# Kernel tuning notes

Measured on AMD Instinct MI355X. Metric: run time of the kernel, lower is better.

## Reference

```python
import jax, jax.numpy as jnp
import numpy as np

H = 4            # num_heads (forced: 128 projection / d_k=32)
DK = 32          # hardcoded d_k
SCALE = 1.0 / np.sqrt(32.0)
EPS = 1e-5       # LayerNorm eps (torch default)


def setup_inputs() -> dict:
    key = jax.random.key(0)
    ks = jax.random.split(key, 8)
    B, L, Dq, Dkv, M = 16, 4096, 512, 512, 512
    def w(k, shape, fan_in):
        return (jax.random.normal(k, shape, jnp.float32) / np.sqrt(fan_in)).astype(jnp.float32)
    return {
        "Q_in":  jax.random.normal(ks[0], (B, L, Dq),  jnp.float32),
        "KV_in": jax.random.normal(ks[1], (B, L, Dkv), jnp.float32),
        "Wq":  w(ks[2], (Dq, 128), Dq),   "bq":  jnp.zeros((128,), jnp.float32),
        "Wk":  w(ks[3], (Dkv, 128), Dkv), "bk":  jnp.zeros((128,), jnp.float32),
        "Wv":  w(ks[4], (Dkv, 128), Dkv), "bv":  jnp.zeros((128,), jnp.float32),
        "Wo":  w(ks[5], (128, M), 128),   "bo":  jnp.zeros((M,), jnp.float32),
        "Wqo": w(ks[6], (128, M), 128),   "bqo": jnp.zeros((M,), jnp.float32),
        "gamma": jnp.ones((M,), jnp.float32),
        "beta":  jnp.zeros((M,), jnp.float32),
    }


def reference(Q_in, KV_in, Wq, bq, Wk, bk, Wv, bv, Wo, bo, Wqo, bqo, gamma, beta):
    B, L, _ = Q_in.shape
    Qm = Q_in @ Wq + bq          # (B, L, 128)
    Km = KV_in @ Wk + bk         # (B, L, 128)
    Vm = KV_in @ Wv + bv         # (B, L, 128)

    def heads(X):
        # view(B, L, H, DK).permute(0, 2, 3, 1) -> (B, H, DK, L)
        return X.reshape(B, L, H, DK).transpose(0, 2, 3, 1)

    Qh, Kh, Vh = heads(Qm), heads(Km), heads(Vm)
    # matmul contracts over the SEQUENCE dim -> feature-feature scores (B,H,DK,DK)
    scores = jnp.einsum('bhdl,bhel->bhde', Qh, Kh) * SCALE
    attn = jax.nn.softmax(scores, axis=-1)          # dropout = identity (eval)
    out_h = jnp.einsum('bhde,bhel->bhdl', attn, Vh)  # (B, H, DK, L)
    out_h = out_h.transpose(0, 3, 1, 2).reshape(B, L, H * DK)  # (B, L, 128)

    out = out_h @ Wo + bo        # (B, L, M)
    Qm_ = Qm @ Wqo + bqo         # (B, L, M)
    x = Qm_ + out
    mu = jnp.mean(x, axis=-1, keepdims=True)
    var = jnp.var(x, axis=-1, keepdims=True)
    y = (x - mu) * jax.lax.rsqrt(var + EPS) * gamma + beta
    return (y, attn)
```

## Files before the change

kernel.cpp:

```cpp
#include <hip/hip_runtime.h>
#include <hip/hip_bf16.h>

typedef __bf16 bf16x8 __attribute__((ext_vector_type(8)));
typedef float  f32x4  __attribute__((ext_vector_type(4)));

#define SCALE_QK 0.17677669529663687f
#define LDSS 40

__device__ __forceinline__ float b2f(ushort u) {
    __hip_bfloat16 h; *reinterpret_cast<ushort*>(&h) = u; return __bfloat162float(h);
}
__device__ __forceinline__ ushort f2b(float f) {
    __hip_bfloat16 h = __float2bfloat16(f); return *reinterpret_cast<ushort*>(&h);
}

__global__ void k_prep(const float* __restrict__ Wq, const float* __restrict__ Wk,
                       const float* __restrict__ Wv, const float* __restrict__ Wqo,
                       const float* __restrict__ Wo,
                       ushort* __restrict__ WqThi, ushort* __restrict__ WqTlo,
                       ushort* __restrict__ WkThi, ushort* __restrict__ WkTlo,
                       ushort* __restrict__ WvT,  ushort* __restrict__ WqoT,
                       ushort* __restrict__ WoB) {
    int idx = blockIdx.x * 256 + threadIdx.x;
    int mat = idx >> 16, i = idx & 65535;
    if (mat == 0) {
        int n = i >> 9, k = i & 511;
        float w = Wq[k * 128 + n];
        ushort hi = f2b(w);
        WqThi[i] = hi; WqTlo[i] = f2b(w - b2f(hi));
    } else if (mat == 1) {
        int n = i >> 9, k = i & 511;
        float w = Wk[k * 128 + n];
        ushort hi = f2b(w);
        WkThi[i] = hi; WkTlo[i] = f2b(w - b2f(hi));
    } else if (mat == 2) {
        int n = i >> 9, k = i & 511;
        WvT[i] = f2b(Wv[k * 128 + n]);
    } else if (mat == 3) {
        int n = i >> 7, k = i & 127;
        WqoT[i] = f2b(Wqo[k * 512 + n]);
    } else if (mat == 4) {
        WoB[i] = f2b(Wo[i]);
    }
}

__global__ __launch_bounds__(256) void k_proj_split(
        const float* __restrict__ A, const ushort* __restrict__ BThi,
        const ushort* __restrict__ BTlo, const float* __restrict__ bias,
        float* __restrict__ outF, ushort* __restrict__ outB) {
    __shared__ __align__(16) ushort AsH[128 * LDSS], AsL[128 * LDSS];
    __shared__ __align__(16) ushort BsH[128 * LDSS], BsL[128 * LDSS];
    const int row0 = blockIdx.x * 128;
    const int tid  = threadIdx.x;
    const int wid  = tid >> 6, lane = tid & 63;
    const int wm = wid >> 1, wn = wid & 1;
    const int quad = lane >> 4, l16 = lane & 15;
    const int sr = tid >> 2;
    const int sc = (tid & 3) * 8;

    f32x4 acc[4][4] = {};

    for (int k0 = 0; k0 < 512; k0 += 32) {
        __syncthreads();
#pragma unroll
        for (int p = 0; p < 2; ++p) {
            int r = sr + p * 64;
            float4 a0 = *(const float4*)&A[(size_t)(row0 + r) * 512 + k0 + sc];
            float4 a1 = *(const float4*)&A[(size_t)(row0 + r) * 512 + k0 + sc + 4];
            float av[8] = {a0.x, a0.y, a0.z, a0.w, a1.x, a1.y, a1.z, a1.w};
            union { uint4 v; ushort u[8]; } H, L;
#pragma unroll
            for (int i = 0; i < 8; ++i) {
                ushort hi = f2b(av[i]);
                H.u[i] = hi;
                L.u[i] = f2b(av[i] - b2f(hi));
            }
            *(uint4*)&AsH[r * LDSS + sc] = H.v;
            *(uint4*)&AsL[r * LDSS + sc] = L.v;
            *(uint4*)&BsH[r * LDSS + sc] = *(const uint4*)&BThi[(size_t)r * 512 + k0 + sc];
            *(uint4*)&BsL[r * LDSS + sc] = *(const uint4*)&BTlo[(size_t)r * 512 + k0 + sc];
        }
        __syncthreads();
        bf16x8 aH[4], aL[4];
#pragma unroll
        for (int i = 0; i < 4; ++i) {
            int ro = (wm * 64 + i * 16 + l16) * LDSS + quad * 8;
            aH[i] = *reinterpret_cast<const bf16x8*>(&AsH[ro]);
            aL[i] = *reinterpret_cast<const bf16x8*>(&AsL[ro]);
        }
#pragma unroll
        for (int j = 0; j < 4; ++j) {
            int ro = (wn * 64 + j * 16 + l16) * LDSS + quad * 8;
            bf16x8 bH = *reinterpret_cast<const bf16x8*>(&BsH[ro]);
            bf16x8 bL = *reinterpret_cast<const bf16x8*>(&BsL[ro]);
#pragma unroll
            for (int i = 0; i < 4; ++i) {
                acc[i][j] = __builtin_amdgcn_mfma_f32_16x16x32_bf16(aL[i], bH, acc[i][j], 0, 0, 0);
                acc[i][j] = __builtin_amdgcn_mfma_f32_16x16x32_bf16(aH[i], bL, acc[i][j], 0, 0, 0);
                acc[i][j] = __builtin_amdgcn_mfma_f32_16x16x32_bf16(aH[i], bH, acc[i][j], 0, 0, 0);
            }
        }
    }

#pragma unroll
    for (int i = 0; i < 4; ++i)
#pragma unroll
        for (int j = 0; j < 4; ++j) {
            int ncol = wn * 64 + j * 16 + l16;
            float bv = bias[ncol];
#pragma unroll
            for (int r = 0; r < 4; ++r) {
                int mrow = row0 + wm * 64 + i * 16 + quad * 4 + r;
                float v = acc[i][j][r] + bv;
                if (outF) outF[(size_t)mrow * 128 + ncol] = v;
                if (outB) outB[(size_t)mrow * 128 + ncol] = f2b(v);
            }
        }
}

__global__ __launch_bounds__(256) void k_proj_kv(
        const float* __restrict__ A,
        const ushort* __restrict__ BKhi, const ushort* __restrict__ BKlo,
        const ushort* __restrict__ BV,
        const float* __restrict__ biasK, const float* __restrict__ biasV,
        float* __restrict__ KmF, ushort* __restrict__ VmB) {
    __shared__ __align__(16) ushort AsH[128 * LDSS], AsL[128 * LDSS];
    __shared__ __align__(16) ushort BsKH[128 * LDSS], BsKL[128 * LDSS], BsV[128 * LDSS];
    const int row0 = blockIdx.x * 128;
    const int tid  = threadIdx.x;
    const int wid  = tid >> 6, lane = tid & 63;
    const int wm = wid >> 1, wn = wid & 1;
    const int quad = lane >> 4, l16 = lane & 15;
    const int sr = tid >> 2;
    const int sc = (tid & 3) * 8;

    f32x4 accK[4][4] = {};
    f32x4 accV[4][4] = {};

    for (int k0 = 0; k0 < 512; k0 += 32) {
        __syncthreads();
#pragma unroll
        for (int p = 0; p < 2; ++p) {
            int r = sr + p * 64;
            float4 a0 = *(const float4*)&A[(size_t)(row0 + r) * 512 + k0 + sc];
            float4 a1 = *(const float4*)&A[(size_t)(row0 + r) * 512 + k0 + sc + 4];
            float av[8] = {a0.x, a0.y, a0.z, a0.w, a1.x, a1.y, a1.z, a1.w};
            union { uint4 v; ushort u[8]; } H, L;
#pragma unroll
            for (int i = 0; i < 8; ++i) {
                ushort hi = f2b(av[i]);
                H.u[i] = hi;
                L.u[i] = f2b(av[i] - b2f(hi));
            }
            *(uint4*)&AsH[r * LDSS + sc] = H.v;
            *(uint4*)&AsL[r * LDSS + sc] = L.v;
            *(uint4*)&BsKH[r * LDSS + sc] = *(const uint4*)&BKhi[(size_t)r * 512 + k0 + sc];
            *(uint4*)&BsKL[r * LDSS + sc] = *(const uint4*)&BKlo[(size_t)r * 512 + k0 + sc];
            *(uint4*)&BsV [r * LDSS + sc] = *(const uint4*)&BV  [(size_t)r * 512 + k0 + sc];
        }
        __syncthreads();
        bf16x8 aH[4], aL[4];
#pragma unroll
        for (int i = 0; i < 4; ++i) {
            int ro = (wm * 64 + i * 16 + l16) * LDSS + quad * 8;
            aH[i] = *reinterpret_cast<const bf16x8*>(&AsH[ro]);
            aL[i] = *reinterpret_cast<const bf16x8*>(&AsL[ro]);
        }
#pragma unroll
        for (int j = 0; j < 4; ++j) {
            int ro = (wn * 64 + j * 16 + l16) * LDSS + quad * 8;
            bf16x8 bKH = *reinterpret_cast<const bf16x8*>(&BsKH[ro]);
            bf16x8 bKL = *reinterpret_cast<const bf16x8*>(&BsKL[ro]);
            bf16x8 bV  = *reinterpret_cast<const bf16x8*>(&BsV [ro]);
#pragma unroll
            for (int i = 0; i < 4; ++i) {
                accK[i][j] = __builtin_amdgcn_mfma_f32_16x16x32_bf16(aL[i], bKH, accK[i][j], 0, 0, 0);
                accK[i][j] = __builtin_amdgcn_mfma_f32_16x16x32_bf16(aH[i], bKL, accK[i][j], 0, 0, 0);
                accK[i][j] = __builtin_amdgcn_mfma_f32_16x16x32_bf16(aH[i], bKH, accK[i][j], 0, 0, 0);
                accV[i][j] = __builtin_amdgcn_mfma_f32_16x16x32_bf16(aH[i], bV,  accV[i][j], 0, 0, 0);
            }
        }
    }

#pragma unroll
    for (int i = 0; i < 4; ++i)
#pragma unroll
        for (int j = 0; j < 4; ++j) {
            int ncol = wn * 64 + j * 16 + l16;
            float bk = biasK[ncol], bv = biasV[ncol];
#pragma unroll
            for (int r = 0; r < 4; ++r) {
                int mrow = row0 + wm * 64 + i * 16 + quad * 4 + r;
                KmF[(size_t)mrow * 128 + ncol] = accK[i][j][r] + bk;
                VmB[(size_t)mrow * 128 + ncol] = f2b(accV[i][j][r] + bv);
            }
        }
}

__global__ __launch_bounds__(256) void k_scores(
        const float* __restrict__ Qm, const float* __restrict__ Km,
        float* __restrict__ partial) {
    int b = blockIdx.x, sp = blockIdx.y;
    int t = threadIdx.x;
    int h = t >> 6, tl = t & 63;
    int d0 = (tl >> 3) * 4, e0 = (tl & 7) * 4;
    const float* Qb = Qm + ((size_t)b * 4096 + sp * 128) * 128 + h * 32 + d0;
    const float* Kb = Km + ((size_t)b * 4096 + sp * 128) * 128 + h * 32 + e0;
    float acc[4][4] = {};
#pragma unroll 4
    for (int l = 0; l < 128; ++l) {
        float4 q4 = *(const float4*)(Qb + (size_t)l * 128);
        float4 k4 = *(const float4*)(Kb + (size_t)l * 128);
        float q[4] = {q4.x, q4.y, q4.z, q4.w};
        float k[4] = {k4.x, k4.y, k4.z, k4.w};
#pragma unroll
        for (int i = 0; i < 4; ++i)
#pragma unroll
            for (int j = 0; j < 4; ++j) acc[i][j] += q[i] * k[j];
    }
    float* P = partial + ((size_t)(sp * 64 + b * 4 + h)) * 1024;
#pragma unroll
    for (int i = 0; i < 4; ++i)
#pragma unroll
        for (int j = 0; j < 4; ++j)
            P[(d0 + i) * 32 + e0 + j] = acc[i][j];
}

__global__ __launch_bounds__(256) void k_attn(
        const float* __restrict__ partial, const ushort* __restrict__ WoB,
        float* __restrict__ attnOut, ushort* __restrict__ WcT) {
    int bh = blockIdx.x; int b = bh >> 2, h = bh & 3;
    __shared__ float aS[1024];
    __shared__ __align__(16) ushort wS[32 * 512];
    int t = threadIdx.x;
    for (int i = t; i < 1024; i += 256) {
        float s = 0.f;
#pragma unroll
        for (int sp = 0; sp < 32; ++sp)
            s += partial[(size_t)(sp * 64 + bh) * 1024 + i];
        aS[i] = s * SCALE_QK;
    }
    for (int i = t; i < 2048; i += 256) {
        int r = i >> 6, c = (i & 63) * 8;
        *(uint4*)&wS[r * 512 + c] = *(const uint4*)&WoB[(size_t)(h * 32 + r) * 512 + c];
    }
    __syncthreads();
    if (t < 32) {
        float m = -1e30f;
#pragma unroll
        for (int e = 0; e < 32; ++e) m = fmaxf(m, aS[t * 32 + e]);
        float p[32]; float sum = 0.f;
#pragma unroll
        for (int e = 0; e < 32; ++e) { p[e] = __expf(aS[t * 32 + e] - m); sum += p[e]; }
        float inv = 1.f / sum;
#pragma unroll
        for (int e = 0; e < 32; ++e) aS[t * 32 + e] = p[e] * inv;
    }
    __syncthreads();
    for (int i = t; i < 1024; i += 256)
        attnOut[(size_t)bh * 1024 + i] = aS[i];
    int e = t & 31, mg = t >> 5;
    for (int mi = 0; mi < 64; ++mi) {
        int m = mg * 64 + mi;
        float acc = 0.f;
#pragma unroll
        for (int d = 0; d < 32; ++d)
            acc += aS[d * 32 + e] * b2f(wS[d * 512 + m]);
        WcT[((size_t)b * 512 + m) * 128 + h * 32 + e] = f2b(acc);
    }
}

__global__ __launch_bounds__(256) void k_out_ln(
        const ushort* __restrict__ Vm, const ushort* __restrict__ Qm,
        const ushort* __restrict__ WcT, const ushort* __restrict__ WqoT,
        const float* __restrict__ bo, const float* __restrict__ bqo,
        const float* __restrict__ gamma, const float* __restrict__ beta,
        float* __restrict__ Y) {
    __shared__ __align__(16) ushort As[64 * LDSS];
    __shared__ __align__(16) ushort Bs[512 * LDSS];
    __shared__ float sumS[4][64], sumSS[4][64], muA[64], rsA[64];
    const int row0 = blockIdx.x * 64;
    const int b = row0 >> 12;
    const ushort* WcTb = WcT + (size_t)b * 512 * 128;
    const int tid = threadIdx.x;
    const int wid = tid >> 6, lane = tid & 63;
    const int quad = lane >> 4, l16 = lane & 15;
    const int sr = tid >> 2;
    const int sc = (tid & 3) * 8;

    f32x4 acc[4][8] = {};

    for (int k0 = 0; k0 < 256; k0 += 32) {
        const ushort* Asrc; const ushort* Bsrc; int kk;
        if (k0 < 128) { Asrc = Vm; Bsrc = WcTb; kk = k0; }
        else          { Asrc = Qm; Bsrc = WqoT; kk = k0 - 128; }
        __syncthreads();
        *(uint4*)&As[sr * LDSS + sc] =
            *(const uint4*)&Asrc[(size_t)(row0 + sr) * 128 + kk + sc];
#pragma unroll
        for (int p = 0; p < 8; ++p) {
            int r = sr + p * 64;
            *(uint4*)&Bs[r * LDSS + sc] = *(const uint4*)&Bsrc[(size_t)r * 128 + kk + sc];
        }
        __syncthreads();
        bf16x8 aF[4];
#pragma unroll
        for (int i = 0; i < 4; ++i)
            aF[i] = *reinterpret_cast<const bf16x8*>(&As[(i * 16 + l16) * LDSS + quad * 8]);
#pragma unroll
        for (int j = 0; j < 8; ++j) {
            bf16x8 bF = *reinterpret_cast<const bf16x8*>(
                &Bs[(wid * 128 + j * 16 + l16) * LDSS + quad * 8]);
#pragma unroll
            for (int i = 0; i < 4; ++i)
                acc[i][j] = __builtin_amdgcn_mfma_f32_16x16x32_bf16(aF[i], bF, acc[i][j], 0, 0, 0);
        }
    }

    float bv[8];
#pragma unroll
    for (int j = 0; j < 8; ++j) {
        int ncol = wid * 128 + j * 16 + l16;
        bv[j] = bo[ncol] + bqo[ncol];
    }
    float sArr[4][4], ssArr[4][4];
#pragma unroll
    for (int i = 0; i < 4; ++i)
#pragma unroll
        for (int r = 0; r < 4; ++r) {
            float s = 0.f, ss = 0.f;
#pragma unroll
            for (int j = 0; j < 8; ++j) {
                float x = acc[i][j][r] + bv[j];
                s += x; ss += x * x;
            }
            sArr[i][r] = s; ssArr[i][r] = ss;
        }
#pragma unroll
    for (int off = 1; off < 16; off <<= 1)
#pragma unroll
        for (int i = 0; i < 4; ++i)
#pragma unroll
            for (int r = 0; r < 4; ++r) {
                sArr[i][r]  += __shfl_xor(sArr[i][r],  off, 64);
                ssArr[i][r] += __shfl_xor(ssArr[i][r], off, 64);
            }
    if (l16 == 0) {
#pragma unroll
        for (int i = 0; i < 4; ++i)
#pragma unroll
            for (int r = 0; r < 4; ++r) {
                int row = i * 16 + quad * 4 + r;
                sumS[wid][row]  = sArr[i][r];
                sumSS[wid][row] = ssArr[i][r];
            }
    }
    __syncthreads();
    if (tid < 64) {
        float s = sumS[0][tid] + sumS[1][tid] + sumS[2][tid] + sumS[3][tid];
        float ss = sumSS[0][tid] + sumSS[1][tid] + sumSS[2][tid] + sumSS[3][tid];
        float mu = s * (1.f / 512.f);
        float var = ss * (1.f / 512.f) - mu * mu;
        muA[tid] = mu;
        rsA[tid] = rsqrtf(var + 1e-5f);
    }
    __syncthreads();

    float gj[8], bj[8];
#pragma unroll
    for (int j = 0; j < 8; ++j) {
        int ncol = wid * 128 + j * 16 + l16;
        gj[j] = gamma[ncol]; bj[j] = beta[ncol];
    }
#pragma unroll
    for (int i = 0; i < 4; ++i)
#pragma unroll
        for (int r = 0; r < 4; ++r) {
            int row = i * 16 + quad * 4 + r;
            float mu = muA[row], rstd = rsA[row];
            size_t base = (size_t)(row0 + row) * 512 + wid * 128 + l16;
#pragma unroll
            for (int j = 0; j < 8; ++j) {
                float x = acc[i][j][r] + bv[j];
                Y[base + j * 16] = (x - mu) * rstd * gj[j] + bj[j];
            }
        }
}

extern "C" void kernel_launch(void* const* d_in, const int* in_sizes, int n_in,
                              void* d_out, int out_size, void* d_ws, size_t ws_size,
                              hipStream_t stream) {
    const float* Qin   = (const float*)d_in[0];
    const float* KVin  = (const float*)d_in[1];
    const float* Wq    = (const float*)d_in[2];
    const float* bq    = (const float*)d_in[3];
    const float* Wk    = (const float*)d_in[4];
    const float* bk    = (const float*)d_in[5];
    const float* Wv    = (const float*)d_in[6];
    const float* bv    = (const float*)d_in[7];
    const float* Wo    = (const float*)d_in[8];
    const float* bo    = (const float*)d_in[9];
    const float* Wqo   = (const float*)d_in[10];
    const float* bqo   = (const float*)d_in[11];
    const float* gamma = (const float*)d_in[12];
    const float* beta  = (const float*)d_in[13];
    float* out = (float*)d_out;
    float* attnOut = out + 33554432;

    char* ws = (char*)d_ws;
    ushort* WqThi = (ushort*)(ws);
    ushort* WqTlo = (ushort*)(ws + 131072);
    ushort* WkThi = (ushort*)(ws + 262144);
    ushort* WkTlo = (ushort*)(ws + 393216);
    ushort* WvT   = (ushort*)(ws + 524288);
    ushort* WqoT  = (ushort*)(ws + 655360);
    ushort* WoB   = (ushort*)(ws + 786432);
    float*  QmF   = (float*) (ws + 917504);
    float*  KmF   = (float*) (ws + 34471936);
    ushort* QmB   = (ushort*)(ws + 68026368);
    ushort* VmB   = (ushort*)(ws + 84803584);
    float*  part  = (float*) (ws + 101580800);
    ushort* WcT   = (ushort*)(ws + 109969408);

    k_prep<<<1280, 256, 0, stream>>>(Wq, Wk, Wv, Wqo, Wo,
                                     WqThi, WqTlo, WkThi, WkTlo, WvT, WqoT, WoB);
    k_proj_split<<<512, 256, 0, stream>>>(Qin, WqThi, WqTlo, bq, QmF, QmB);
    k_proj_kv<<<512, 256, 0, stream>>>(KVin, WkThi, WkTlo, WvT, bk, bv, KmF, VmB);
    k_scores<<<dim3(16, 32), 256, 0, stream>>>(QmF, KmF, part);
    k_attn<<<64, 256, 0, stream>>>(part, WoB, attnOut, WcT);
    k_out_ln<<<1024, 256, 0, stream>>>(VmB, QmB, WcT, WqoT, bo, bqo, gamma, beta, out);
}
```

Before: 488.7 us.

## Fuse Q/KV projections with score computation and switch split-bf16 to fp16 MFMA

Merges the Q projection, K/V projection and per-chunk QK^T score kernels into one kernel. Q and K tiles now stay in LDS as fp16 and feed MFMA score products directly, so the fp32 Qm/Km intermediates are no longer written to or read back from global memory. The three-term split-bf16 emulation of fp32 GEMMs is replaced with a single fp16 MFMA per tile, cutting matrix instructions and LDS staging. The cost is lower precision from fp16 inputs, with possible overflow or accuracy loss, and higher LDS use per block.

```diff
diff --git a/kernel.cpp b/kernel.cpp
--- a/kernel.cpp
+++ b/kernel.cpp
@@ -1,41 +1,41 @@
 #include <hip/hip_runtime.h>
 #include <hip/hip_bf16.h>
 
-typedef __bf16 bf16x8 __attribute__((ext_vector_type(8)));
-typedef float  f32x4  __attribute__((ext_vector_type(4)));
+typedef __bf16   bf16x8 __attribute__((ext_vector_type(8)));
+typedef _Float16 f16x8  __attribute__((ext_vector_type(8)));
+typedef float    f32x4  __attribute__((ext_vector_type(4)));
 
 #define SCALE_QK 0.17677669529663687f
 #define LDSS 40
+#define TL   136
 
 __device__ __forceinline__ float b2f(ushort u) {
     __hip_bfloat16 h; *reinterpret_cast<ushort*>(&h) = u; return __bfloat162float(h);
 }
 __device__ __forceinline__ ushort f2b(float f) {
     __hip_bfloat16 h = __float2bfloat16(f); return *reinterpret_cast<ushort*>(&h);
+}
+__device__ __forceinline__ ushort f2h(float f) {
+    union { _Float16 h; ushort u; } x; x.h = (_Float16)f; return x.u;
 }
 
 __global__ void k_prep(const float* __restrict__ Wq, const float* __restrict__ Wk,
                        const float* __restrict__ Wv, const float* __restrict__ Wqo,
                        const float* __restrict__ Wo,
-                       ushort* __restrict__ WqThi, ushort* __restrict__ WqTlo,
-                       ushort* __restrict__ WkThi, ushort* __restrict__ WkTlo,
-                       ushort* __restrict__ WvT,  ushort* __restrict__ WqoT,
+                       ushort* __restrict__ WqT, ushort* __restrict__ WkT,
+                       ushort* __restrict__ WvT, ushort* __restrict__ WqoT,
                        ushort* __restrict__ WoB) {
     int idx = blockIdx.x * 256 + threadIdx.x;
     int mat = idx >> 16, i = idx & 65535;
     if (mat == 0) {
         int n = i >> 9, k = i & 511;
-        float w = Wq[k * 128 + n];
-        ushort hi = f2b(w);
-        WqThi[i] = hi; WqTlo[i] = f2b(w - b2f(hi));
+        WqT[i] = f2h(Wq[k * 128 + n]);
     } else if (mat == 1) {
         int n = i >> 9, k = i & 511;
-        float w = Wk[k * 128 + n];
-        ushort hi = f2b(w);
-        WkThi[i] = hi; WkTlo[i] = f2b(w - b2f(hi));
+        WkT[i] = f2h(Wk[k * 128 + n]);
     } else if (mat == 2) {
         int n = i >> 9, k = i & 511;
-        WvT[i] = f2b(Wv[k * 128 + n]);
+        WvT[i] = f2h(Wv[k * 128 + n]);
     } else if (mat == 3) {
         int n = i >> 7, k = i & 127;
         WqoT[i] = f2b(Wqo[k * 512 + n]);
@@ -44,12 +44,21 @@
     }
 }
 
-__global__ __launch_bounds__(256) void k_proj_split(
-        const float* __restrict__ A, const ushort* __restrict__ BThi,
-        const ushort* __restrict__ BTlo, const float* __restrict__ bias,
-        float* __restrict__ outF, ushort* __restrict__ outB) {
-    __shared__ __align__(16) ushort AsH[128 * LDSS], AsL[128 * LDSS];
-    __shared__ __align__(16) ushort BsH[128 * LDSS], BsL[128 * LDSS];
+__global__ __launch_bounds__(256) void k_qkv_scores(
+        const float* __restrict__ Qin, const float* __restrict__ KVin,
+        const ushort* __restrict__ WqT, const ushort* __restrict__ WkT,
+        const ushort* __restrict__ WvT,
+        const float* __restrict__ bq, const float* __restrict__ bk,
+        const float* __restrict__ bv,
+        ushort* __restrict__ QmB, ushort* __restrict__ VmB,
+        float* __restrict__ partial) {
+    __shared__ __align__(16) ushort lds[2 * 128 * TL];
+    ushort* P1  = lds;
+    ushort* P2  = lds + 128 * TL;
+    ushort* As  = P2;
+    ushort* Bs0 = P2 + 128 * LDSS;
+    ushort* Bs1 = P2 + 2 * 128 * LDSS;
+
     const int row0 = blockIdx.x * 128;
     const int tid  = threadIdx.x;
     const int wid  = tid >> 6, lane = tid & 63;
@@ -58,172 +67,133 @@
     const int sr = tid >> 2;
     const int sc = (tid & 3) * 8;
 
-    f32x4 acc[4][4] = {};
-
-    for (int k0 = 0; k0 < 512; k0 += 32) {
+    {
+        f32x4 acc[4][4] = {};
+        for (int k0 = 0; k0 < 512; k0 += 32) {
+            __syncthreads();
+#pragma unroll
+            for (int p = 0; p < 2; ++p) {
+                int r = sr + p * 64;
+                float4 a0 = *(const float4*)&Qin[(size_t)(row0 + r) * 512 + k0 + sc];
+                float4 a1 = *(const float4*)&Qin[(size_t)(row0 + r) * 512 + k0 + sc + 4];
+                union { uint4 v; ushort u[8]; } H;
+                H.u[0] = f2h(a0.x); H.u[1] = f2h(a0.y); H.u[2] = f2h(a0.z); H.u[3] = f2h(a0.w);
+                H.u[4] = f2h(a1.x); H.u[5] = f2h(a1.y); H.u[6] = f2h(a1.z); H.u[7] = f2h(a1.w);
+                *(uint4*)&As[r * LDSS + sc]  = H.v;
+                *(uint4*)&Bs0[r * LDSS + sc] = *(const uint4*)&WqT[(size_t)r * 512 + k0 + sc];
+            }
+            __syncthreads();
+            f16x8 aF[4];
+#pragma unroll
+            for (int i = 0; i < 4; ++i)
+                aF[i] = *reinterpret_cast<const f16x8*>(&As[(wm * 64 + i * 16 + l16) * LDSS + quad * 8]);
+#pragma unroll
+            for (int j = 0; j < 4; ++j) {
+                f16x8 bF = *reinterpret_cast<const f16x8*>(&Bs0[(wn * 64 + j * 16 + l16) * LDSS + quad * 8]);
+#pragma unroll
+                for (int i = 0; i < 4; ++i)
+                    acc[i][j] = __builtin_amdgcn_mfma_f32_16x16x32_f16(aF[i], bF, acc[i][j], 0, 0, 0);
+            }
+        }
+#pragma unroll
+        for (int j = 0; j < 4; ++j) {
+            int col = wn * 64 + j * 16 + l16;
+            float bqv = bq[col];
+#pragma unroll
+            for (int i = 0; i < 4; ++i)
+#pragma unroll
+                for (int r = 0; r < 4; ++r) {
+                    int row = wm * 64 + i * 16 + quad * 4 + r;
+                    float v = acc[i][j][r] + bqv;
+                    QmB[(size_t)(row0 + row) * 128 + col] = f2b(v);
+                    P1[col * TL + row] = f2h(v);
+                }
+        }
+    }
+
+    {
+        f32x4 accK[4][4] = {};
+        f32x4 accV[4][4] = {};
+        for (int k0 = 0; k0 < 512; k0 += 32) {
+            __syncthreads();
+#pragma unroll
+            for (int p = 0; p < 2; ++p) {
+                int r = sr + p * 64;
+                float4 a0 = *(const float4*)&KVin[(size_t)(row0 + r) * 512 + k0 + sc];
+                float4 a1 = *(const float4*)&KVin[(size_t)(row0 + r) * 512 + k0 + sc + 4];
+                union { uint4 v; ushort u[8]; } H;
+                H.u[0] = f2h(a0.x); H.u[1] = f2h(a0.y); H.u[2] = f2h(a0.z); H.u[3] = f2h(a0.w);
+                H.u[4] = f2h(a1.x); H.u[5] = f2h(a1.y); H.u[6] = f2h(a1.z); H.u[7] = f2h(a1.w);
+                *(uint4*)&As[r * LDSS + sc]  = H.v;
+                *(uint4*)&Bs0[r * LDSS + sc] = *(const uint4*)&WkT[(size_t)r * 512 + k0 + sc];
+                *(uint4*)&Bs1[r * LDSS + sc] = *(const uint4*)&WvT[(size_t)r * 512 + k0 + sc];
+            }
+            __syncthreads();
+            f16x8 aF[4];
+#pragma unroll
+            for (int i = 0; i < 4; ++i)
+                aF[i] = *reinterpret_cast<const f16x8*>(&As[(wm * 64 + i * 16 + l16) * LDSS + quad * 8]);
+#pragma unroll
+            for (int j = 0; j < 4; ++j) {
+                f16x8 bK = *reinterpret_cast<const f16x8*>(&Bs0[(wn * 64 + j * 16 + l16) * LDSS + quad * 8]);
+                f16x8 bV = *reinterpret_cast<const f16x8*>(&Bs1[(wn * 64 + j * 16 + l16) * LDSS + quad * 8]);
+#pragma unroll
+                for (int i = 0; i < 4; ++i) {
+                    accK[i][j] = __builtin_amdgcn_mfma_f32_16x16x32_f16(aF[i], bK, accK[i][j], 0, 0, 0);
+                    accV[i][j] = __builtin_amdgcn_mfma_f32_16x16x32_f16(aF[i], bV, accV[i][j], 0, 0, 0);
+                }
+            }
+        }
         __syncthreads();
 #pragma unroll
-        for (int p = 0; p < 2; ++p) {
-            int r = sr + p * 64;
-            float4 a0 = *(const float4*)&A[(size_t)(row0 + r) * 512 + k0 + sc];
-            float4 a1 = *(const float4*)&A[(size_t)(row0 + r) * 512 + k0 + sc + 4];
-            float av[8] = {a0.x, a0.y, a0.z, a0.w, a1.x, a1.y, a1.z, a1.w};
-            union { uint4 v; ushort u[8]; } H, L;
-#pragma unroll
-            for (int i = 0; i < 8; ++i) {
-                ushort hi = f2b(av[i]);
-                H.u[i] = hi;
-                L.u[i] = f2b(av[i] - b2f(hi));
-            }
-            *(uint4*)&AsH[r * LDSS + sc] = H.v;
-            *(uint4*)&AsL[r * LDSS + sc] = L.v;
-            *(uint4*)&BsH[r * LDSS + sc] = *(const uint4*)&BThi[(size_t)r * 512 + k0 + sc];
-            *(uint4*)&BsL[r * LDSS + sc] = *(const uint4*)&BTlo[(size_t)r * 512 + k0 + sc];
-        }
-        __syncthreads();
-        bf16x8 aH[4], aL[4];
-#pragma unroll
-        for (int i = 0; i < 4; ++i) {
-            int ro = (wm * 64 + i * 16 + l16) * LDSS + quad * 8;
-            aH[i] = *reinterpret_cast<const bf16x8*>(&AsH[ro]);
-            aL[i] = *reinterpret_cast<const bf16x8*>(&AsL[ro]);
-        }
-#pragma unroll
         for (int j = 0; j < 4; ++j) {
-            int ro = (wn * 64 + j * 16 + l16) * LDSS + quad * 8;
-            bf16x8 bH = *reinterpret_cast<const bf16x8*>(&BsH[ro]);
-            bf16x8 bL = *reinterpret_cast<const bf16x8*>(&BsL[ro]);
-#pragma unroll
-            for (int i = 0; i < 4; ++i) {
-                acc[i][j] = __builtin_amdgcn_mfma_f32_16x16x32_bf16(aL[i], bH, acc[i][j], 0, 0, 0);
-                acc[i][j] = __builtin_amdgcn_mfma_f32_16x16x32_bf16(aH[i], bL, acc[i][j], 0, 0, 0);
-                acc[i][j] = __builtin_amdgcn_mfma_f32_16x16x32_bf16(aH[i], bH, acc[i][j], 0, 0, 0);
-            }
-        }
-    }
-
-#pragma unroll
-    for (int i = 0; i < 4; ++i)
-#pragma unroll
-        for (int j = 0; j < 4; ++j) {
-            int ncol = wn * 64 + j * 16 + l16;
-            float bv = bias[ncol];
-#pragma unroll
-            for (int r = 0; r < 4; ++r) {
-                int mrow = row0 + wm * 64 + i * 16 + quad * 4 + r;
-                float v = acc[i][j][r] + bv;
-                if (outF) outF[(size_t)mrow * 128 + ncol] = v;
-                if (outB) outB[(size_t)mrow * 128 + ncol] = f2b(v);
-            }
-        }
-}
-
-__global__ __launch_bounds__(256) void k_proj_kv(
-        const float* __restrict__ A,
-        const ushort* __restrict__ BKhi, const ushort* __restrict__ BKlo,
-        const ushort* __restrict__ BV,
-        const float* __restrict__ biasK, const float* __restrict__ biasV,
-        float* __restrict__ KmF, ushort* __restrict__ VmB) {
-    __shared__ __align__(16) ushort AsH[128 * LDSS], AsL[128 * LDSS];
-    __shared__ __align__(16) ushort BsKH[128 * LDSS], BsKL[128 * LDSS], BsV[128 * LDSS];
-    const int row0 = blockIdx.x * 128;
-    const int tid  = threadIdx.x;
-    const int wid  = tid >> 6, lane = tid & 63;
-    const int wm = wid >> 1, wn = wid & 1;
-    const int quad = lane >> 4, l16 = lane & 15;
-    const int sr = tid >> 2;
-    const int sc = (tid & 3) * 8;
-
-    f32x4 accK[4][4] = {};
-    f32x4 accV[4][4] = {};
-
-    for (int k0 = 0; k0 < 512; k0 += 32) {
-        __syncthreads();
-#pragma unroll
-        for (int p = 0; p < 2; ++p) {
-            int r = sr + p * 64;
-            float4 a0 = *(const float4*)&A[(size_t)(row0 + r) * 512 + k0 + sc];
-            float4 a1 = *(const float4*)&A[(size_t)(row0 + r) * 512 + k0 + sc + 4];
-            float av[8] = {a0.x, a0.y, a0.z, a0.w, a1.x, a1.y, a1.z, a1.w};
-            union { uint4 v; ushort u[8]; } H, L;
-#pragma unroll
-            for (int i = 0; i < 8; ++i) {
-                ushort hi = f2b(av[i]);
-                H.u[i] = hi;
-                L.u[i] = f2b(av[i] - b2f(hi));
-            }
-            *(uint4*)&AsH[r * LDSS + sc] = H.v;
-            *(uint4*)&AsL[r * LDSS + sc] = L.v;
-            *(uint4*)&BsKH[r * LDSS + sc] = *(const uint4*)&BKhi[(size_t)r * 512 + k0 + sc];
-            *(uint4*)&BsKL[r * LDSS + sc] = *(const uint4*)&BKlo[(size_t)r * 512 + k0 + sc];
-            *(uint4*)&BsV [r * LDSS + sc] = *(const uint4*)&BV  [(size_t)r * 512 + k0 + sc];
-        }
-        __syncthreads();
-        bf16x8 aH[4], aL[4];
-#pragma unroll
-        for (int i = 0; i < 4; ++i) {
-            int ro = (wm * 64 + i * 16 + l16) * LDSS + quad * 8;
-            aH[i] = *reinterpret_cast<const bf16x8*>(&AsH[ro]);
-            aL[i] = *reinterpret_cast<const bf16x8*>(&AsL[ro]);
-        }
-#pragma unroll
-        for (int j = 0; j < 4; ++j) {
-            int ro = (wn * 64 + j * 16 + l16) * LDSS + quad * 8;
-            bf16x8 bKH = *reinterpret_cast<const bf16x8*>(&BsKH[ro]);
-            bf16x8 bKL = *reinterpret_cast<const bf16x8*>(&BsKL[ro]);
-            bf16x8 bV  = *reinterpret_cast<const bf16x8*>(&BsV [ro]);
-#pragma unroll
-            for (int i = 0; i < 4; ++i) {
-                accK[i][j] = __builtin_amdgcn_mfma_f32_16x16x32_bf16(aL[i], bKH, accK[i][j], 0, 0, 0);
-                accK[i][j] = __builtin_amdgcn_mfma_f32_16x16x32_bf16(aH[i], bKL, accK[i][j], 0, 0, 0);
-                accK[i][j] = __builtin_amdgcn_mfma_f32_16x16x32_bf16(aH[i], bKH, accK[i][j], 0, 0, 0);
-                accV[i][j] = __builtin_amdgcn_mfma_f32_16x16x32_bf16(aH[i], bV,  accV[i][j], 0, 0, 0);
-            }
-        }
-    }
-
-#pragma unroll
-    for (int i = 0; i < 4; ++i)
-#pragma unroll
-        for (int j = 0; j < 4; ++j) {
-            int ncol = wn * 64 + j * 16 + l16;
-            float bk = biasK[ncol], bv = biasV[ncol];
-#pragma unroll
-            for (int r = 0; r < 4; ++r) {
-                int mrow = row0 + wm * 64 + i * 16 + quad * 4 + r;
-                KmF[(size_t)mrow * 128 + ncol] = accK[i][j][r] + bk;
-                VmB[(size_t)mrow * 128 + ncol] = f2b(accV[i][j][r] + bv);
-            }
-        }
-}
-
-__global__ __launch_bounds__(256) void k_scores(
-        const float* __restrict__ Qm, const float* __restrict__ Km,
-        float* __restrict__ partial) {
-    int b = blockIdx.x, sp = blockIdx.y;
-    int t = threadIdx.x;
-    int h = t >> 6, tl = t & 63;
-    int d0 = (tl >> 3) * 4, e0 = (tl & 7) * 4;
-    const float* Qb = Qm + ((size_t)b * 4096 + sp * 128) * 128 + h * 32 + d0;
-    const float* Kb = Km + ((size_t)b * 4096 + sp * 128) * 128 + h * 32 + e0;
-    float acc[4][4] = {};
-#pragma unroll 4
-    for (int l = 0; l < 128; ++l) {
-        float4 q4 = *(const float4*)(Qb + (size_t)l * 128);
-        float4 k4 = *(const float4*)(Kb + (size_t)l * 128);
-        float q[4] = {q4.x, q4.y, q4.z, q4.w};
-        float k[4] = {k4.x, k4.y, k4.z, k4.w};
-#pragma unroll
-        for (int i = 0; i < 4; ++i)
-#pragma unroll
-            for (int j = 0; j < 4; ++j) acc[i][j] += q[i] * k[j];
-    }
-    float* P = partial + ((size_t)(sp * 64 + b * 4 + h)) * 1024;
-#pragma unroll
-    for (int i = 0; i < 4; ++i)
-#pragma unroll
-        for (int j = 0; j < 4; ++j)
-            P[(d0 + i) * 32 + e0 + j] = acc[i][j];
+            int col = wn * 64 + j * 16 + l16;
+            float bkv = bk[col], bvv = bv[col];
+#pragma unroll
+            for (int i = 0; i < 4; ++i)
+#pragma unroll
+                for (int r = 0; r < 4; ++r) {
+                    int row = wm * 64 + i * 16 + quad * 4 + r;
+                    float vv = accV[i][j][r] + bvv;
+                    VmB[(size_t)(row0 + row) * 128 + col] = f2b(vv);
+                    P2[col * TL + row] = f2h(accK[i][j][r] + bkv);
+                }
+        }
+    }
+    __syncthreads();
+
+    {
+        const int h = wid;
+        f32x4 s[2][2] = {};
+#pragma unroll
+        for (int ks = 0; ks < 4; ++ks) {
+            f16x8 qa[2], kb[2];
+#pragma unroll
+            for (int dt = 0; dt < 2; ++dt)
+                qa[dt] = *reinterpret_cast<const f16x8*>(
+                    &P1[(h * 32 + dt * 16 + l16) * TL + ks * 32 + quad * 8]);
+#pragma unroll
+            for (int et = 0; et < 2; ++et)
+                kb[et] = *reinterpret_cast<const f16x8*>(
+                    &P2[(h * 32 + et * 16 + l16) * TL + ks * 32 + quad * 8]);
+#pragma unroll
+            for (int dt = 0; dt < 2; ++dt)
+#pragma unroll
+                for (int et = 0; et < 2; ++et)
+                    s[dt][et] = __builtin_amdgcn_mfma_f32_16x16x32_f16(qa[dt], kb[et], s[dt][et], 0, 0, 0);
+        }
+        const int b = blockIdx.x >> 5, sp = blockIdx.x & 31;
+        float* P = partial + (size_t)(sp * 64 + b * 4 + h) * 1024;
+#pragma unroll
+        for (int dt = 0; dt < 2; ++dt)
+#pragma unroll
+            for (int et = 0; et < 2; ++et)
+#pragma unroll
+                for (int r = 0; r < 4; ++r) {
+                    int d = dt * 16 + quad * 4 + r, e = et * 16 + l16;
+                    P[d * 32 + e] = s[dt][et][r];
+                }
+    }
 }
 
 __global__ __launch_bounds__(256) void k_attn(
@@ -408,25 +378,20 @@
     float* attnOut = out + 33554432;
 
     char* ws = (char*)d_ws;
-    ushort* WqThi = (ushort*)(ws);
-    ushort* WqTlo = (ushort*)(ws + 131072);
-    ushort* WkThi = (ushort*)(ws + 262144);
-    ushort* WkTlo = (ushort*)(ws + 393216);
-    ushort* WvT   = (ushort*)(ws + 524288);
-    ushort* WqoT  = (ushort*)(ws + 655360);
-    ushort* WoB   = (ushort*)(ws + 786432);
-    float*  QmF   = (float*) (ws + 917504);
-    float*  KmF   = (float*) (ws + 34471936);
-    ushort* QmB   = (ushort*)(ws + 68026368);
-    ushort* VmB   = (ushort*)(ws + 84803584);
-    float*  part  = (float*) (ws + 101580800);
-    ushort* WcT   = (ushort*)(ws + 109969408);
+    ushort* WqT  = (ushort*)(ws);
+    ushort* WkT  = (ushort*)(ws + 131072);
+    ushort* WvT  = (ushort*)(ws + 262144);
+    ushort* WqoT = (ushort*)(ws + 393216);
+    ushort* WoB  = (ushort*)(ws + 524288);
+    ushort* QmB  = (ushort*)(ws + 655360);
+    ushort* VmB  = (ushort*)(ws + 17432576);
+    float*  part = (float*) (ws + 34209792);
+    ushort* WcT  = (ushort*)(ws + 42598400);
 
     k_prep<<<1280, 256, 0, stream>>>(Wq, Wk, Wv, Wqo, Wo,
-                                     WqThi, WqTlo, WkThi, WkTlo, WvT, WqoT, WoB);
-    k_proj_split<<<512, 256, 0, stream>>>(Qin, WqThi, WqTlo, bq, QmF, QmB);
-    k_proj_kv<<<512, 256, 0, stream>>>(KVin, WkThi, WkTlo, WvT, bk, bv, KmF, VmB);
-    k_scores<<<dim3(16, 32), 256, 0, stream>>>(QmF, KmF, part);
+                                     WqT, WkT, WvT, WqoT, WoB);
+    k_qkv_scores<<<512, 256, 0, stream>>>(Qin, KVin, WqT, WkT, WvT,
+                                          bq, bk, bv, QmB, VmB, part);
     k_attn<<<64, 256, 0, stream>>>(part, WoB, attnOut, WcT);
     k_out_ln<<<1024, 256, 0, stream>>>(VmB, QmB, WcT, WqoT, bo, bqo, gamma, beta, out);
 }
```

Result: faster. 434.5 us (-11.1%).
